# Kernel optimization log

Hardware: AMD Instinct MI355X
Metric: run time of the kernel (lower is better)

The kernel has to match this reference:

```python
import jax, jax.numpy as jnp
import numpy as np

N_NODES = 100000
N_EDGES = 1600000
IN_F = 128
H_F = 128
N_CLS = 8
N_LAYERS = 6


def setup_inputs() -> dict:
    key = jax.random.key(0)
    ks = jax.random.split(key, 8)
    scale = 1.0 / np.sqrt(H_F)
    return {
        "in_feat": jax.random.normal(ks[0], (N_NODES, IN_F), dtype=jnp.float32),
        "src": jax.random.randint(ks[1], (N_EDGES,), 0, N_NODES, dtype=jnp.int32),
        "dst": jax.random.randint(ks[2], (N_EDGES,), 0, N_NODES, dtype=jnp.int32),
        "edge_weight": jax.random.uniform(ks[3], (N_EDGES,), dtype=jnp.float32),
        "conv_W": jax.random.normal(ks[4], (N_LAYERS, H_F, H_F), dtype=jnp.float32) * scale,
        "conv_b": jnp.zeros((N_LAYERS, H_F), dtype=jnp.float32),
        "lin_W": jax.random.normal(ks[5], (H_F, N_CLS), dtype=jnp.float32) * scale,
        "lin_b": jnp.zeros((N_CLS,), dtype=jnp.float32),
    }


def _degree_norms(src, dst, n):
    ones = jnp.ones(src.shape[0], dtype=jnp.float32)
    out_deg = jax.ops.segment_sum(ones, src, num_segments=n)
    in_deg = jax.ops.segment_sum(ones, dst, num_segments=n)
    # DGL norm='both': clamp degrees to min 1, then ^-0.5 (structural degrees)
    norm_src = jnp.power(jnp.maximum(out_deg, 1.0), -0.5)[:, None]  # [N,1]
    norm_dst = jnp.power(jnp.maximum(in_deg, 1.0), -0.5)[:, None]   # [N,1]
    return norm_src, norm_dst


def _graph_conv(x, W, b, src, dst, ew, norm_src, norm_dst):
    # linear commutes with (linear) aggregation; apply weight first
    h = (x @ W) * norm_src                     # [N,F]
    msg = h[src] * ew[:, None]                 # [E,F] gather * edge weight
    agg = jax.ops.segment_sum(msg, dst, num_segments=x.shape[0])
    return agg * norm_dst + b


def reference(in_feat, src, dst, edge_weight, conv_W, conv_b, lin_W, lin_b):
    norm_src, norm_dst = _degree_norms(src, dst, in_feat.shape[0])
    h = in_feat
    for i in range(N_LAYERS):
        h = jax.nn.leaky_relu(
            _graph_conv(h, conv_W[i], conv_b[i], src, dst, edge_weight, norm_src, norm_dst),
            negative_slope=0.01,
        )
    return h @ lin_W + lin_b
```

## Files before the change

kernel.cpp:

```cpp
#include <hip/hip_runtime.h>
#include <math.h>

#define N_NODES 100000
#define N_EDGES 1600000
#define HF 128
#define N_CLS 8
#define N_LAYERS 6
#define TILE_N 64
#define SCAN_B 1024
#define SCAN_NB ((N_NODES + SCAN_B - 1) / SCAN_B)
#define HBINS 8192
#define HCHUNK ((N_NODES + HBINS - 1) / HBINS)
#define HSLICE 8

__global__ void deg_rank_kernel(const int* __restrict__ dst,
                                int* __restrict__ ind, int* __restrict__ rank) {
    int e = blockIdx.x * blockDim.x + threadIdx.x;
    if (e < N_EDGES) {
        rank[e] = atomicAdd(&ind[dst[e]], 1);
    }
}

__global__ __launch_bounds__(1024) void outdeg_hist_kernel(const int* __restrict__ src,
                                                           int* __restrict__ outd) {
    __shared__ int hist[HBINS];
    int chunk = blockIdx.x;
    int slice = blockIdx.y;
    int lo = chunk * HBINS;
    int hi = lo + HBINS;
    for (int i = threadIdx.x; i < HBINS; i += 1024) hist[i] = 0;
    __syncthreads();
    const int4* s4 = (const int4*)src;
    const int n4 = N_EDGES / 4;
    int per = (n4 + HSLICE - 1) / HSLICE;
    int beg = slice * per;
    int end = beg + per; if (end > n4) end = n4;
    for (int i = beg + threadIdx.x; i < end; i += 1024) {
        int4 v = s4[i];
        if (v.x >= lo && v.x < hi) atomicAdd(&hist[v.x - lo], 1);
        if (v.y >= lo && v.y < hi) atomicAdd(&hist[v.y - lo], 1);
        if (v.z >= lo && v.z < hi) atomicAdd(&hist[v.z - lo], 1);
        if (v.w >= lo && v.w < hi) atomicAdd(&hist[v.w - lo], 1);
    }
    __syncthreads();
    for (int i = threadIdx.x; i < HBINS; i += 1024) {
        int c = hist[i];
        if (c != 0 && lo + i < N_NODES) atomicAdd(&outd[lo + i], c);
    }
}

__global__ void norm_kernel(const int* __restrict__ outd, const int* __restrict__ ind,
                            float* __restrict__ ns, float* __restrict__ nd) {
    int n = blockIdx.x * blockDim.x + threadIdx.x;
    if (n < N_NODES) {
        int od = outd[n]; if (od < 1) od = 1;
        int id = ind[n];  if (id < 1) id = 1;
        ns[n] = rsqrtf((float)od);
        nd[n] = rsqrtf((float)id);
    }
}

__global__ __launch_bounds__(SCAN_B) void scan1_kernel(const int* __restrict__ deg,
                                                       int* __restrict__ incl,
                                                       int* __restrict__ bsum) {
    __shared__ int buf[SCAN_B];
    int t = threadIdx.x;
    int g = blockIdx.x * SCAN_B + t;
    int v = (g < N_NODES) ? deg[g] : 0;
    buf[t] = v;
    __syncthreads();
    #pragma unroll
    for (int off = 1; off < SCAN_B; off <<= 1) {
        int add = (t >= off) ? buf[t - off] : 0;
        __syncthreads();
        buf[t] += add;
        __syncthreads();
    }
    if (g < N_NODES) incl[g] = buf[t];
    if (t == SCAN_B - 1) bsum[blockIdx.x] = buf[t];
}

__global__ __launch_bounds__(128) void scan2_kernel(int* __restrict__ bsum) {
    __shared__ int buf[128];
    int t = threadIdx.x;
    buf[t] = (t < SCAN_NB) ? bsum[t] : 0;
    __syncthreads();
    #pragma unroll
    for (int off = 1; off < 128; off <<= 1) {
        int add = (t >= off) ? buf[t - off] : 0;
        __syncthreads();
        buf[t] += add;
        __syncthreads();
    }
    if (t < SCAN_NB) bsum[t] = buf[t];
}

__global__ __launch_bounds__(SCAN_B) void scan3_kernel(const int* __restrict__ deg,
                                                       const int* __restrict__ incl,
                                                       const int* __restrict__ bsum,
                                                       int* __restrict__ row_ptr) {
    int t = threadIdx.x;
    int g = blockIdx.x * SCAN_B + t;
    if (g < N_NODES) {
        int off = (blockIdx.x > 0) ? bsum[blockIdx.x - 1] : 0;
        row_ptr[g] = off + incl[g] - deg[g];
    }
    if (g == 0) row_ptr[N_NODES] = bsum[SCAN_NB - 1];
}

__global__ void scatter2_kernel(const int* __restrict__ src, const int* __restrict__ dst,
                                const float* __restrict__ ew, const float* __restrict__ ns,
                                const float* __restrict__ nd, const int* __restrict__ row_ptr,
                                const int* __restrict__ rank, float2* __restrict__ esw) {
    int e = blockIdx.x * blockDim.x + threadIdx.x;
    if (e < N_EDGES) {
        int s = src[e];
        int d = dst[e];
        int pos = row_ptr[d] + rank[e];
        esw[pos] = make_float2(__int_as_float(s), ew[e] * ns[s] * nd[d]);
    }
}

__global__ __launch_bounds__(256) void gemm_kernel(const float* __restrict__ X,
                                                   const float* __restrict__ W,
                                                   float* __restrict__ Y) {
    __shared__ float Xs[TILE_N][HF];
    int tid = threadIdx.x;
    int nodeBase = blockIdx.x * TILE_N;

    for (int i = tid; i < TILE_N * (HF / 4); i += 256) {
        int r = i >> 5;
        int c = i & 31;
        int n = nodeBase + r;
        float4 v = make_float4(0.f, 0.f, 0.f, 0.f);
        if (n < N_NODES) v = ((const float4*)(X + (size_t)n * HF))[c];
        ((float4*)(&Xs[r][0]))[c] = v;
    }
    __syncthreads();

    int tx = tid & 31;
    int ty = tid >> 5;

    float acc[8][4];
    #pragma unroll
    for (int i = 0; i < 8; i++)
        #pragma unroll
        for (int j = 0; j < 4; j++) acc[i][j] = 0.f;

    const float4* W4 = (const float4*)W;

    for (int k4 = 0; k4 < HF / 4; k4++) {
        float4 wv0 = W4[(k4 * 4 + 0) * 32 + tx];
        float4 wv1 = W4[(k4 * 4 + 1) * 32 + tx];
        float4 wv2 = W4[(k4 * 4 + 2) * 32 + tx];
        float4 wv3 = W4[(k4 * 4 + 3) * 32 + tx];
        #pragma unroll
        for (int i = 0; i < 8; i++) {
            float4 xv = ((const float4*)(&Xs[ty + 8 * i][0]))[k4];
            acc[i][0] += xv.x * wv0.x; acc[i][1] += xv.x * wv0.y;
            acc[i][2] += xv.x * wv0.z; acc[i][3] += xv.x * wv0.w;
            acc[i][0] += xv.y * wv1.x; acc[i][1] += xv.y * wv1.y;
            acc[i][2] += xv.y * wv1.z; acc[i][3] += xv.y * wv1.w;
            acc[i][0] += xv.z * wv2.x; acc[i][1] += xv.z * wv2.y;
            acc[i][2] += xv.z * wv2.z; acc[i][3] += xv.z * wv2.w;
            acc[i][0] += xv.w * wv3.x; acc[i][1] += xv.w * wv3.y;
            acc[i][2] += xv.w * wv3.z; acc[i][3] += xv.w * wv3.w;
        }
    }

    #pragma unroll
    for (int i = 0; i < 8; i++) {
        int n = nodeBase + ty + 8 * i;
        if (n < N_NODES) {
            float4 o = make_float4(acc[i][0], acc[i][1], acc[i][2], acc[i][3]);
            ((float4*)(Y + (size_t)n * HF))[tx] = o;
        }
    }
}

__global__ __launch_bounds__(256) void agg_kernel(const float* __restrict__ hl,
                                                  const int* __restrict__ row_ptr,
                                                  const float2* __restrict__ esw,
                                                  const float* __restrict__ bias,
                                                  float* __restrict__ out) {
    int node = blockIdx.x * 4 + (threadIdx.x >> 6);
    if (node >= N_NODES) return;
    int lane = threadIdx.x & 63;

    int beg = row_ptr[node];
    int end = row_ptr[node + 1];
    float ax = 0.f, ay = 0.f;

    for (int i = beg; i < end; i += 8) {
        float2 p[8];
        #pragma unroll
        for (int j = 0; j < 8; j++) {
            p[j] = (i + j < end) ? esw[i + j] : make_float2(__int_as_float(0), 0.f);
        }
        float2 v[8];
        #pragma unroll
        for (int j = 0; j < 8; j++) {
            int s = __float_as_int(p[j].x);
            v[j] = ((const float2*)(hl + (size_t)s * HF))[lane];
        }
        #pragma unroll
        for (int j = 0; j < 8; j++) {
            ax += v[j].x * p[j].y;
            ay += v[j].y * p[j].y;
        }
    }
    float2 bb = ((const float2*)bias)[lane];
    float ox = ax + bb.x;
    float oy = ay + bb.y;
    ox = (ox > 0.f) ? ox : 0.01f * ox;
    oy = (oy > 0.f) ? oy : 0.01f * oy;
    ((float2*)(out + (size_t)node * HF))[lane] = make_float2(ox, oy);
}

__global__ __launch_bounds__(256) void proj_kernel(const float* __restrict__ h,
                                                   const float* __restrict__ W,
                                                   const float* __restrict__ b,
                                                   float* __restrict__ out) {
    int node = blockIdx.x * (blockDim.x >> 6) + (threadIdx.x >> 6);
    if (node >= N_NODES) return;
    int lane = threadIdx.x & 63;

    float2 v = *(const float2*)(h + (size_t)node * HF + lane * 2);
    float acc[N_CLS];
    #pragma unroll
    for (int c = 0; c < N_CLS; c++) {
        acc[c] = v.x * W[(lane * 2) * N_CLS + c] + v.y * W[(lane * 2 + 1) * N_CLS + c];
    }
    #pragma unroll
    for (int off = 32; off > 0; off >>= 1) {
        #pragma unroll
        for (int c = 0; c < N_CLS; c++) acc[c] += __shfl_down(acc[c], off);
    }
    if (lane == 0) {
        #pragma unroll
        for (int c = 0; c < N_CLS; c++) out[(size_t)node * N_CLS + c] = acc[c] + b[c];
    }
}

extern "C" void kernel_launch(void* const* d_in, const int* in_sizes, int n_in,
                              void* d_out, int out_size, void* d_ws, size_t ws_size,
                              hipStream_t stream) {
    const float* in_feat = (const float*)d_in[0];
    const int*   src     = (const int*)d_in[1];
    const int*   dst     = (const int*)d_in[2];
    const float* ew      = (const float*)d_in[3];
    const float* conv_W  = (const float*)d_in[4];
    const float* conv_b  = (const float*)d_in[5];
    const float* lin_W   = (const float*)d_in[6];
    const float* lin_b   = (const float*)d_in[7];
    float* out = (float*)d_out;

    char* p = (char*)d_ws;
    float* hA = (float*)p;        p += (size_t)N_NODES * HF * sizeof(float);
    float* hB = (float*)p;        p += (size_t)N_NODES * HF * sizeof(float);
    float2* esw = (float2*)p;     p += (size_t)N_EDGES * sizeof(float2);
    int*   row_ptr = (int*)p;     p += ((size_t)N_NODES + 8) * sizeof(int);
    int*   out_deg = (int*)p;     p += (size_t)N_NODES * sizeof(int);
    int*   in_deg = (int*)p;      p += (size_t)N_NODES * sizeof(int);
    float* norm_src = (float*)p;  p += (size_t)N_NODES * sizeof(float);
    float* norm_dst = (float*)p;  p += (size_t)N_NODES * sizeof(float);
    int*   incl = (int*)p;        p += (size_t)N_NODES * sizeof(int);
    int*   bsum = (int*)p;        p += 256 * sizeof(int);
    int*   rank = (int*)hB;
    (void)p; (void)ws_size; (void)in_sizes; (void)n_in; (void)out_size;

    hipMemsetAsync(out_deg, 0, (size_t)N_NODES * sizeof(int), stream);
    hipMemsetAsync(in_deg, 0, (size_t)N_NODES * sizeof(int), stream);

    int egrid = (N_EDGES + 255) / 256;
    int ngrid = (N_NODES + 255) / 256;

    deg_rank_kernel<<<egrid, 256, 0, stream>>>(dst, in_deg, rank);
    outdeg_hist_kernel<<<dim3(HCHUNK, HSLICE), 1024, 0, stream>>>(src, out_deg);
    norm_kernel<<<ngrid, 256, 0, stream>>>(out_deg, in_deg, norm_src, norm_dst);
    scan1_kernel<<<SCAN_NB, SCAN_B, 0, stream>>>(in_deg, incl, bsum);
    scan2_kernel<<<1, 128, 0, stream>>>(bsum);
    scan3_kernel<<<SCAN_NB, SCAN_B, 0, stream>>>(in_deg, incl, bsum, row_ptr);
    scatter2_kernel<<<egrid, 256, 0, stream>>>(src, dst, ew, norm_src, norm_dst,
                                               row_ptr, rank, esw);

    int ggrid = (N_NODES + TILE_N - 1) / TILE_N;
    int agrid = (N_NODES + 3) / 4;

    const float* cur = in_feat;
    for (int l = 0; l < N_LAYERS; l++) {
        gemm_kernel<<<ggrid, 256, 0, stream>>>(cur, conv_W + (size_t)l * HF * HF, hB);
        agg_kernel<<<agrid, 256, 0, stream>>>(hB, row_ptr, esw,
                                              conv_b + (size_t)l * HF, hA);
        cur = hA;
    }
    proj_kernel<<<agrid, 256, 0, stream>>>(hA, lin_W, lin_b, out);
}
```

Baseline: 1.381 ms.

## Retile GEMM to 4x8 outputs per thread and reduce aggregation unroll to two

```diff
diff --git a/kernel.cpp b/kernel.cpp
--- a/kernel.cpp
+++ b/kernel.cpp
@@ -124,56 +124,74 @@
 __global__ __launch_bounds__(256) void gemm_kernel(const float* __restrict__ X,
                                                    const float* __restrict__ W,
                                                    float* __restrict__ Y) {
-    __shared__ float Xs[TILE_N][HF];
+    __shared__ float Xs[TILE_N][HF + 4];
     int tid = threadIdx.x;
     int nodeBase = blockIdx.x * TILE_N;
 
-    for (int i = tid; i < TILE_N * (HF / 4); i += 256) {
-        int r = i >> 5;
-        int c = i & 31;
+    for (int idx = tid; idx < TILE_N * (HF / 4); idx += 256) {
+        int r = idx >> 5;
+        int c = idx & 31;
         int n = nodeBase + r;
         float4 v = make_float4(0.f, 0.f, 0.f, 0.f);
         if (n < N_NODES) v = ((const float4*)(X + (size_t)n * HF))[c];
-        ((float4*)(&Xs[r][0]))[c] = v;
-    }
-    __syncthreads();
-
-    int tx = tid & 31;
-    int ty = tid >> 5;
-
-    float acc[8][4];
-    #pragma unroll
-    for (int i = 0; i < 8; i++)
-        #pragma unroll
-        for (int j = 0; j < 4; j++) acc[i][j] = 0.f;
+        *(float4*)(&Xs[r][c * 4]) = v;
+    }
+    __syncthreads();
+
+    int tx = tid & 15;
+    int ty = tid >> 4;
+
+    float acc[4][8];
+    #pragma unroll
+    for (int i = 0; i < 4; i++)
+        #pragma unroll
+        for (int j = 0; j < 8; j++) acc[i][j] = 0.f;
 
     const float4* W4 = (const float4*)W;
 
+    #pragma unroll 2
     for (int k4 = 0; k4 < HF / 4; k4++) {
-        float4 wv0 = W4[(k4 * 4 + 0) * 32 + tx];
-        float4 wv1 = W4[(k4 * 4 + 1) * 32 + tx];
-        float4 wv2 = W4[(k4 * 4 + 2) * 32 + tx];
-        float4 wv3 = W4[(k4 * 4 + 3) * 32 + tx];
-        #pragma unroll
-        for (int i = 0; i < 8; i++) {
-            float4 xv = ((const float4*)(&Xs[ty + 8 * i][0]))[k4];
-            acc[i][0] += xv.x * wv0.x; acc[i][1] += xv.x * wv0.y;
-            acc[i][2] += xv.x * wv0.z; acc[i][3] += xv.x * wv0.w;
-            acc[i][0] += xv.y * wv1.x; acc[i][1] += xv.y * wv1.y;
-            acc[i][2] += xv.y * wv1.z; acc[i][3] += xv.y * wv1.w;
-            acc[i][0] += xv.z * wv2.x; acc[i][1] += xv.z * wv2.y;
-            acc[i][2] += xv.z * wv2.z; acc[i][3] += xv.z * wv2.w;
-            acc[i][0] += xv.w * wv3.x; acc[i][1] += xv.w * wv3.y;
-            acc[i][2] += xv.w * wv3.z; acc[i][3] += xv.w * wv3.w;
+        float4 w0[4], w1[4];
+        #pragma unroll
+        for (int kk = 0; kk < 4; kk++) {
+            w0[kk] = W4[(k4 * 4 + kk) * 32 + tx];
+            w1[kk] = W4[(k4 * 4 + kk) * 32 + 16 + tx];
         }
-    }
-
-    #pragma unroll
-    for (int i = 0; i < 8; i++) {
-        int n = nodeBase + ty + 8 * i;
+        float4 xv[4];
+        #pragma unroll
+        for (int i = 0; i < 4; i++)
+            xv[i] = *(const float4*)(&Xs[ty + 16 * i][k4 * 4]);
+        #pragma unroll
+        for (int i = 0; i < 4; i++) {
+            acc[i][0] += xv[i].x * w0[0].x; acc[i][1] += xv[i].x * w0[0].y;
+            acc[i][2] += xv[i].x * w0[0].z; acc[i][3] += xv[i].x * w0[0].w;
+            acc[i][4] += xv[i].x * w1[0].x; acc[i][5] += xv[i].x * w1[0].y;
+            acc[i][6] += xv[i].x * w1[0].z; acc[i][7] += xv[i].x * w1[0].w;
+
+            acc[i][0] += xv[i].y * w0[1].x; acc[i][1] += xv[i].y * w0[1].y;
+            acc[i][2] += xv[i].y * w0[1].z; acc[i][3] += xv[i].y * w0[1].w;
+            acc[i][4] += xv[i].y * w1[1].x; acc[i][5] += xv[i].y * w1[1].y;
+            acc[i][6] += xv[i].y * w1[1].z; acc[i][7] += xv[i].y * w1[1].w;
+
+            acc[i][0] += xv[i].z * w0[2].x; acc[i][1] += xv[i].z * w0[2].y;
+            acc[i][2] += xv[i].z * w0[2].z; acc[i][3] += xv[i].z * w0[2].w;
+            acc[i][4] += xv[i].z * w1[2].x; acc[i][5] += xv[i].z * w1[2].y;
+            acc[i][6] += xv[i].z * w1[2].z; acc[i][7] += xv[i].z * w1[2].w;
+
+            acc[i][0] += xv[i].w * w0[3].x; acc[i][1] += xv[i].w * w0[3].y;
+            acc[i][2] += xv[i].w * w0[3].z; acc[i][3] += xv[i].w * w0[3].w;
+            acc[i][4] += xv[i].w * w1[3].x; acc[i][5] += xv[i].w * w1[3].y;
+            acc[i][6] += xv[i].w * w1[3].z; acc[i][7] += xv[i].w * w1[3].w;
+        }
+    }
+
+    #pragma unroll
+    for (int i = 0; i < 4; i++) {
+        int n = nodeBase + ty + 16 * i;
         if (n < N_NODES) {
-            float4 o = make_float4(acc[i][0], acc[i][1], acc[i][2], acc[i][3]);
-            ((float4*)(Y + (size_t)n * HF))[tx] = o;
+            float4* yrow = (float4*)(Y + (size_t)n * HF);
+            yrow[tx]      = make_float4(acc[i][0], acc[i][1], acc[i][2], acc[i][3]);
+            yrow[16 + tx] = make_float4(acc[i][4], acc[i][5], acc[i][6], acc[i][7]);
         }
     }
 }
@@ -190,24 +208,22 @@
     int beg = row_ptr[node];
     int end = row_ptr[node + 1];
     float ax = 0.f, ay = 0.f;
-
-    for (int i = beg; i < end; i += 8) {
-        float2 p[8];
-        #pragma unroll
-        for (int j = 0; j < 8; j++) {
-            p[j] = (i + j < end) ? esw[i + j] : make_float2(__int_as_float(0), 0.f);
-        }
-        float2 v[8];
-        #pragma unroll
-        for (int j = 0; j < 8; j++) {
-            int s = __float_as_int(p[j].x);
-            v[j] = ((const float2*)(hl + (size_t)s * HF))[lane];
-        }
-        #pragma unroll
-        for (int j = 0; j < 8; j++) {
-            ax += v[j].x * p[j].y;
-            ay += v[j].y * p[j].y;
-        }
+    int i = beg;
+    for (; i + 2 <= end; i += 2) {
+        float2 p0 = esw[i];
+        float2 p1 = esw[i + 1];
+        int s0 = __float_as_int(p0.x);
+        int s1 = __float_as_int(p1.x);
+        float2 v0 = ((const float2*)(hl + (size_t)s0 * HF))[lane];
+        float2 v1 = ((const float2*)(hl + (size_t)s1 * HF))[lane];
+        ax += v0.x * p0.y; ay += v0.y * p0.y;
+        ax += v1.x * p1.y; ay += v1.y * p1.y;
+    }
+    if (i < end) {
+        float2 p = esw[i];
+        int s = __float_as_int(p.x);
+        float2 v = ((const float2*)(hl + (size_t)s * HF))[lane];
+        ax += v.x * p.y; ay += v.y * p.y;
     }
     float2 bb = ((const float2*)bias)[lane];
     float ox = ax + bb.x;
```

Result: slower. 1.417 ms (+2.6%).
